# Kernel optimization log

Hardware: AMD Instinct MI355X
Metric: run time of the kernel (lower is better)

The kernel has to match this reference:

```python
import jax, jax.numpy as jnp
import numpy as np

B, IN_CAPS, IN_DIM = 64, 2048, 16
NUM_CAPS, OUT_DIM = 32, 16
NUM_ROUTING = 3


def squash(v, axis=-1):
    # scale = |v|^2 / (1 + |v|^2) / |v|  (faithful to source, no epsilon)
    s2 = jnp.sum(jnp.square(v), axis=axis, keepdims=True)
    scale = s2 / (1.0 + s2) / jnp.sqrt(s2)
    return scale * v


def setup_inputs() -> dict:
    key = jax.random.key(0)
    k1, k2 = jax.random.split(key)
    inputs = jax.random.normal(k1, (B, IN_CAPS, IN_DIM), dtype=jnp.float32)
    # glorot-ish scaled transform matrices
    W = jax.random.normal(k2, (IN_CAPS, NUM_CAPS, IN_DIM, OUT_DIM), dtype=jnp.float32) * 0.05
    return {"inputs": inputs, "W": W}


def reference(inputs, W):
    # Prediction vectors u_hat[b,i,k,:] = inputs[b,i,:] @ W[i,k,:,:]
    u_hat = jnp.einsum('bid,ikdo->biko', inputs, W)  # [B, I, K, O]
    # Routing logits b (per-batch; source initializes from zeros and accumulates agreement)
    b = jnp.zeros(u_hat.shape[:3], dtype=u_hat.dtype)  # [B, I, K]
    v = None
    for i in range(NUM_ROUTING):
        c = jax.nn.softmax(b, axis=2)                      # coupling coeffs over output caps K
        s = jnp.einsum('bik,biko->bko', c, u_hat)          # weighted sum over input caps I
        v = squash(s)                                      # [B, K, O]
        if i != NUM_ROUTING - 1:
            b = b + jnp.einsum('biko,bko->bik', u_hat, v)  # agreement update
    return v  # [B, NUM_CAPS, OUT_DIM]
```

## Files before the change

kernel.cpp:

```cpp
#include <hip/hip_runtime.h>
#include <math.h>
#include <stdint.h>

#define NB 64
#define NI 2048
#define NK 32
#define ND 16

typedef _Float16 h2t   __attribute__((ext_vector_type(2)));
typedef _Float16 f16x4 __attribute__((ext_vector_type(4)));
typedef float    f32x4 __attribute__((ext_vector_type(4)));

#if defined(__has_builtin)
#if __has_builtin(__builtin_amdgcn_global_load_lds)
#define HAVE_GLL 1
#endif
#endif
#ifndef HAVE_GLL
#define HAVE_GLL 0
#endif

static __device__ __forceinline__ uint32_t pack_h2(float a, float b) {
    h2t p; p.x = (_Float16)a; p.y = (_Float16)b;
    return __builtin_bit_cast(uint32_t, p);
}

static __device__ __forceinline__ float swz_xor16(float x) {
    int v = __builtin_amdgcn_ds_swizzle(__builtin_bit_cast(int, x), 0x401F);
    return __builtin_bit_cast(float, v);
}
static __device__ __forceinline__ float xreduce_o(float p) {
    p += swz_xor16(p);
    p += __shfl_xor(p, 32);
    return p;
}

__global__ __launch_bounds__(256)
void conv_w(const float* __restrict__ Wg, uint32_t* __restrict__ Wh)
{
    __shared__ float tile[32 * 264];
    const int i = blockIdx.x;
    const int t = threadIdx.x;
    const float4* src = (const float4*)(Wg + (size_t)i * 8192);
#pragma unroll
    for (int j = 0; j < 8; ++j) {
        const int f4 = t + j * 256;
        const int k  = f4 >> 6;
        const int r4 = f4 & 63;
        *(float4*)(&tile[k * 264 + r4 * 4]) = src[f4];
    }
    __syncthreads();
    const int T  = t >> 3;
    const int l0 = (t & 7) * 8;
    const float* s = tile + T * 264;
    uint2* dst = (uint2*)(Wh + (size_t)i * 4096) + T * 64 + l0;
#pragma unroll
    for (int n = 0; n < 8; ++n) {
        const int l = l0 + n;
        const int q = l >> 4, r = l & 15;
        uint2 u;
        u.x = pack_h2(s[(4 * q + 0) * 16 + r], s[(4 * q + 1) * 16 + r]);
        u.y = pack_h2(s[(4 * q + 2) * 16 + r], s[(4 * q + 3) * 16 + r]);
        dst[n] = u;
    }
}

__global__ __launch_bounds__(256)
void conv_x(const float* __restrict__ X, uint32_t* __restrict__ XT)
{
    const int g = blockIdx.x * 256 + threadIdx.x;
    const int b = g >> 11, i = g & 2047;
    const float4* src = (const float4*)(X + ((size_t)b * 2048 + i) * 16);
    const float4 f0 = src[0], f1 = src[1], f2 = src[2], f3 = src[3];
    uint4 o0, o1;
    o0.x = pack_h2(f0.x, f0.y); o0.y = pack_h2(f0.z, f0.w);
    o0.z = pack_h2(f1.x, f1.y); o0.w = pack_h2(f1.z, f1.w);
    o1.x = pack_h2(f2.x, f2.y); o1.y = pack_h2(f2.z, f2.w);
    o1.z = pack_h2(f3.x, f3.y); o1.w = pack_h2(f3.z, f3.w);
    uint4* dst = (uint4*)(XT + (size_t)i * 512 + b * 8);
    dst[0] = o0; dst[1] = o1;
}

template<int VMODE>
__global__ __launch_bounds__(256, 3)
void caps_pass_m(const uint32_t* __restrict__ XT,
                 const uint32_t* __restrict__ Wh,
                 const float* __restrict__ V,
                 float* __restrict__ part)
{
    constexpr int IC = 8;
    __shared__ uint32_t Ws[3][4096];
    __shared__ uint32_t Xs[1024];
    __shared__ float    Ep[2][4][16];

    const int t = threadIdx.x;
    const int l = t & 63;
    const int w = t >> 6;
    const int r = l & 15;
    const int q = l >> 4;

    const int wg     = blockIdx.x;
    const int xcd    = wg & 7;
    const int slot   = wg >> 3;
    const int ichunk = xcd * 32 + (slot >> 2);
    const int bg     = slot & 3;
    const int i0 = ichunk * IC;
    const int b0 = bg * 16;

    f32x4 s_acc[8];
#pragma unroll
    for (int tt = 0; tt < 8; ++tt) s_acc[tt] = (f32x4){0.f, 0.f, 0.f, 0.f};

    f32x4 v_r[8];
    if constexpr (VMODE == 1) {
#pragma unroll
        for (int tt = 0; tt < 8; ++tt)
            v_r[tt] = *(const f32x4*)(V + ((size_t)(b0 + r) * NK + (8 * w + tt)) * 16 + 4 * q);
    }

    {
        const int ig = t >> 5, uu = t & 31;
        uint4 v = *(const uint4*)(XT + (size_t)(i0 + ig) * 512 + b0 * 8 + uu * 4);
        *(uint4*)&Xs[ig * 128 + uu * 4] = v;
    }

#define STAGE_W(buf, tile)                                                     \
    {                                                                          \
        const size_t ibase_ = (size_t)(tile) * 4096;                           \
        _Pragma("unroll")                                                      \
        for (int j = 0; j < 4; ++j) {                                          \
            const int p = w * 4 + j;                                           \
            STAGE_ONE(buf, ibase_, p)                                          \
        }                                                                      \
    }
#if HAVE_GLL
#define STAGE_ONE(buf, ibase_, p)                                              \
    __builtin_amdgcn_global_load_lds(                                          \
        (const __attribute__((address_space(1))) void*)(Wh + ibase_ + (p) * 256 + l * 4), \
        (__attribute__((address_space(3))) void*)&Ws[buf][(p) * 256], 16, 0, 0);
#define BAR_W(n) asm volatile("s_waitcnt vmcnt(" #n ")\ns_barrier" ::: "memory");
#else
#define STAGE_ONE(buf, ibase_, p)                                              \
    ((uint4*)&Ws[buf][(p) * 256])[l] = *(const uint4*)(Wh + ibase_ + (p) * 256 + l * 4);
#define BAR_W(n) asm volatile("s_waitcnt vmcnt(0) lgkmcnt(0)\ns_barrier" ::: "memory");
#endif
#define BAR_E() asm volatile("s_waitcnt lgkmcnt(0)\ns_barrier" ::: "memory");

    __syncthreads();

    STAGE_W(0, i0)
    STAGE_W(1, i0 + 1)

    int cur = 0;
    for (int ii = 0; ii < IC; ++ii) {
        if (ii + 1 < IC) { BAR_W(4) } else { BAR_W(0) }

        if (ii + 2 < IC) {
            const int nslot = (cur + 2 >= 3) ? cur - 1 : cur + 2;
            STAGE_W(nslot, i0 + ii + 2)
        }

        const f16x4 xb = *(const f16x4*)&Xs[ii * 128 + r * 8 + q * 2];

        if constexpr (VMODE == 0) {
#pragma unroll
            for (int tt = 0; tt < 8; ++tt) {
                const f16x4 a = *(const f16x4*)&Ws[cur][(w * 8 + tt) * 128 + l * 2];
                s_acc[tt] = __builtin_amdgcn_mfma_f32_16x16x16f16(a, xb, s_acc[tt], 0, 0, 0);
            }
        } else {
            f32x4 um[8];
#pragma unroll
            for (int tt = 0; tt < 8; ++tt) {
                const f16x4 a = *(const f16x4*)&Ws[cur][(w * 8 + tt) * 128 + l * 2];
                um[tt] = __builtin_amdgcn_mfma_f32_16x16x16f16(
                    a, xb, (f32x4){0.f, 0.f, 0.f, 0.f}, 0, 0, 0);
            }
            float e[8];
            float esp = 0.f;
#pragma unroll
            for (int tt = 0; tt < 8; ++tt) {
                float p = um[tt][0] * v_r[tt][0];
                p = fmaf(um[tt][1], v_r[tt][1], p);
                p = fmaf(um[tt][2], v_r[tt][2], p);
                p = fmaf(um[tt][3], v_r[tt][3], p);
                p = xreduce_o(p);
                e[tt] = __expf(p);
                esp += e[tt];
            }
            if (q == 0) Ep[ii & 1][w][r] = esp;
            BAR_E();
            const float es = Ep[ii & 1][0][r] + Ep[ii & 1][1][r]
                           + Ep[ii & 1][2][r] + Ep[ii & 1][3][r];
            const float ci = __builtin_amdgcn_rcpf(es);
#pragma unroll
            for (int tt = 0; tt < 8; ++tt) {
                const float c = e[tt] * ci;
                s_acc[tt][0] = fmaf(c, um[tt][0], s_acc[tt][0]);
                s_acc[tt][1] = fmaf(c, um[tt][1], s_acc[tt][1]);
                s_acc[tt][2] = fmaf(c, um[tt][2], s_acc[tt][2]);
                s_acc[tt][3] = fmaf(c, um[tt][3], s_acc[tt][3]);
            }
        }
        cur = (cur == 2) ? 0 : cur + 1;
    }
#undef STAGE_W
#undef STAGE_ONE
#undef BAR_W
#undef BAR_E

    float* base = part + (size_t)(bg * 256 + ichunk) * 8192 + r * 512 + 4 * q;
#pragma unroll
    for (int tt = 0; tt < 8; ++tt) {
        float4 st = {s_acc[tt][0], s_acc[tt][1], s_acc[tt][2], s_acc[tt][3]};
        *(float4*)(base + (8 * w + tt) * 16) = st;
    }
}

template<int RMODE>
__global__ __launch_bounds__(256)
void caps_reduce(const float* __restrict__ part,
                 const float* __restrict__ S0red,
                 float* __restrict__ S0out,
                 float* __restrict__ Vout)
{
    __shared__ float red[4][64];
    const int t   = threadIdx.x;
    const int jl  = t & 63;
    const int qc  = t >> 6;
    const int jb  = blockIdx.x * 64;
    const int j   = jb + jl;
    const int bg  = j >> 13;
    const int loc = j & 8191;
    const float* p = part + ((size_t)(bg * 256 + qc * 64)) * 8192 + loc;
    float sum = 0.f;
#pragma unroll 8
    for (int ic = 0; ic < 64; ++ic) sum += p[(size_t)ic * 8192];
    red[qc][jl] = sum;
    __syncthreads();
    if (t < 64) {
        const int jj = jb + t;
        float total = red[0][t] + red[1][t] + red[2][t] + red[3][t];
        if constexpr (RMODE == 0) {
            S0out[jj] = total;
            float val = total * (1.0f / 32.0f);
            float sq = val * val;
#pragma unroll
            for (int mask = 8; mask >= 1; mask >>= 1) sq += __shfl_xor(sq, mask);
            const float sc = sqrtf(sq) / (1.0f + sq);
            Vout[jj] = val * sc;
        } else if constexpr (RMODE == 1) {
            float val0 = S0red[jj] * (1.0f / 32.0f);
            float sq0 = val0 * val0;
#pragma unroll
            for (int mask = 8; mask >= 1; mask >>= 1) sq0 += __shfl_xor(sq0, mask);
            const float sc0 = sqrtf(sq0) / (1.0f + sq0);
            float sq1 = total * total;
#pragma unroll
            for (int mask = 8; mask >= 1; mask >>= 1) sq1 += __shfl_xor(sq1, mask);
            const float sc1 = sqrtf(sq1) / (1.0f + sq1);
            Vout[jj] = fmaf(val0, sc0, total * sc1);
        } else {
            float sq = total * total;
#pragma unroll
            for (int mask = 8; mask >= 1; mask >>= 1) sq += __shfl_xor(sq, mask);
            const float sc = sqrtf(sq) / (1.0f + sq);
            Vout[jj] = total * sc;
        }
    }
}

template<int VMODE>
__global__ __launch_bounds__(256, 4)
void caps_pass_f32(const float* __restrict__ X,
                   const float* __restrict__ Wg,
                   const float* __restrict__ S0,
                   const float* __restrict__ S1,
                   float* __restrict__ Sout)
{
    constexpr int IC = 8;
    __shared__ float Ws[8192];
    __shared__ float Xs[2048];

    const int t   = threadIdx.x;
    const int kk  = t & 31;
    const int oh  = (t >> 5) & 1;
    const int bq4 = t >> 6;

    const int wg     = blockIdx.x;
    const int xcd    = wg & 7;
    const int slot   = wg >> 3;
    const int ichunk = xcd * 32 + (slot >> 2);
    const int bg     = slot & 3;
    const int i0 = ichunk * IC;
    const int b0 = bg * 16;

    float s_acc[4][8];
#pragma unroll
    for (int bb = 0; bb < 4; ++bb)
#pragma unroll
        for (int o = 0; o < 8; ++o) s_acc[bb][o] = 0.f;

    float v_r[4][8];
    if constexpr (VMODE >= 1) {
#pragma unroll
        for (int bb = 0; bb < 4; ++bb) {
            const int b = b0 + bq4 * 4 + bb;
            const float* p0 = S0 + ((size_t)b * NK + kk) * 16 + oh * 8;
            float4 a = *(const float4*)(p0);
            float4 c = *(const float4*)(p0 + 4);
            float val0[8] = {a.x,a.y,a.z,a.w,c.x,c.y,c.z,c.w};
            float sq0 = 0.f;
#pragma unroll
            for (int o = 0; o < 8; ++o) { val0[o] *= (1.0f/32.0f); sq0 = fmaf(val0[o], val0[o], sq0); }
            sq0 += __shfl_xor(sq0, 32);
            const float sc0 = sqrtf(sq0) / (1.0f + sq0);
#pragma unroll
            for (int o = 0; o < 8; ++o) v_r[bb][o] = val0[o] * sc0;
            if constexpr (VMODE == 2) {
                const float* p1 = S1 + ((size_t)b * NK + kk) * 16 + oh * 8;
                float4 a1 = *(const float4*)(p1);
                float4 c1 = *(const float4*)(p1 + 4);
                float val1[8] = {a1.x,a1.y,a1.z,a1.w,c1.x,c1.y,c1.z,c1.w};
                float sq1 = 0.f;
#pragma unroll
                for (int o = 0; o < 8; ++o) sq1 = fmaf(val1[o], val1[o], sq1);
                sq1 += __shfl_xor(sq1, 32);
                const float sc1 = sqrtf(sq1) / (1.0f + sq1);
#pragma unroll
                for (int o = 0; o < 8; ++o) v_r[bb][o] = fmaf(val1[o], sc1, v_r[bb][o]);
            }
        }
    }

    {
        const int xb   = t >> 4;
        const int xig  = t & 7;
        const int half = (t >> 3) & 1;
        const float* xp = X + (size_t)(b0 + xb) * (NI * ND) + (size_t)(i0 + xig) * ND + half * 8;
        float4 f0 = *(const float4*)(xp);
        float4 f1 = *(const float4*)(xp + 4);
        float vals[8] = {f0.x,f0.y,f0.z,f0.w,f1.x,f1.y,f1.z,f1.w};
        const int m = (xig & 7) << 3;
#pragma unroll
        for (int jj = 0; jj < 8; ++jj) {
            const int d = half * 8 + jj;
            Xs[xig * 256 + ((16 * d + xb) ^ m)] = vals[jj];
        }
    }

    for (int ii = 0; ii < IC; ++ii) {
        const int i = i0 + ii;
        __syncthreads();
        {
            const float4* wsrc = (const float4*)(Wg + (size_t)i * 8192);
#pragma unroll
            for (int j = 0; j < 8; ++j) {
                float4 val = wsrc[t + j * 256];
                const int k = (t >> 6) + 4 * j;
                ((float4*)Ws)[k * 64 + ((t & 63) ^ (k & 7))] = val;
            }
        }
        __syncthreads();

        const int xm = (ii & 7) << 3;
        float u[4][8];
        if constexpr (VMODE >= 1) {
#pragma unroll
            for (int bb = 0; bb < 4; ++bb)
#pragma unroll
                for (int o = 0; o < 8; ++o) u[bb][o] = 0.f;
        }
#pragma unroll
        for (int d = 0; d < 16; ++d) {
            const float4 x4 = *(const float4*)(&Xs[ii * 256 + ((16 * d + 4 * bq4) ^ xm)]);
            float wvv[8];
            {
                const float4 wA = ((const float4*)Ws)[kk * 64 + ((d * 4 + oh * 2)     ^ (kk & 7))];
                const float4 wB = ((const float4*)Ws)[kk * 64 + ((d * 4 + oh * 2 + 1) ^ (kk & 7))];
                wvv[0]=wA.x; wvv[1]=wA.y; wvv[2]=wA.z; wvv[3]=wA.w;
                wvv[4]=wB.x; wvv[5]=wB.y; wvv[6]=wB.z; wvv[7]=wB.w;
            }
            if constexpr (VMODE >= 1) {
#pragma unroll
                for (int o = 0; o < 8; ++o) {
                    u[0][o] = fmaf(x4.x, wvv[o], u[0][o]);
                    u[1][o] = fmaf(x4.y, wvv[o], u[1][o]);
                    u[2][o] = fmaf(x4.z, wvv[o], u[2][o]);
                    u[3][o] = fmaf(x4.w, wvv[o], u[3][o]);
                }
            } else {
#pragma unroll
                for (int o = 0; o < 8; ++o) {
                    s_acc[0][o] = fmaf(x4.x, wvv[o], s_acc[0][o]);
                    s_acc[1][o] = fmaf(x4.y, wvv[o], s_acc[1][o]);
                    s_acc[2][o] = fmaf(x4.z, wvv[o], s_acc[2][o]);
                    s_acc[3][o] = fmaf(x4.w, wvv[o], s_acc[3][o]);
                }
            }
        }

        if constexpr (VMODE >= 1) {
#pragma unroll
            for (int bb = 0; bb < 4; ++bb) {
                float lg = 0.f;
#pragma unroll
                for (int o = 0; o < 8; ++o) lg = fmaf(u[bb][o], v_r[bb][o], lg);
                lg += __shfl_xor(lg, 32);
                float m = lg;
#pragma unroll
                for (int mask = 16; mask >= 1; mask >>= 1)
                    m = fmaxf(m, __shfl_xor(m, mask));
                const float e = __expf(lg - m);
                float ssum = e;
#pragma unroll
                for (int mask = 16; mask >= 1; mask >>= 1)
                    ssum += __shfl_xor(ssum, mask);
                const float c = e / ssum;
#pragma unroll
                for (int o = 0; o < 8; ++o)
                    s_acc[bb][o] = fmaf(c, u[bb][o], s_acc[bb][o]);
            }
        }
    }

#pragma unroll
    for (int bb = 0; bb < 4; ++bb) {
        float* sp = Sout + ((size_t)(b0 + bq4 * 4 + bb) * NK + kk) * 16 + oh * 8;
#pragma unroll
        for (int o = 0; o < 8; ++o) atomicAdd(sp + o, s_acc[bb][o]);
    }
}

__global__ __launch_bounds__(256)
void squash_kernel(const float* __restrict__ S, float* __restrict__ Vout)
{
    const int idx = blockIdx.x * 256 + threadIdx.x;
    float val = S[idx];
    float sq = val * val;
#pragma unroll
    for (int mask = 8; mask >= 1; mask >>= 1) sq += __shfl_xor(sq, mask);
    const float sc = sqrtf(sq) / (1.0f + sq);
    Vout[idx] = val * sc;
}

extern "C" void kernel_launch(void* const* d_in, const int* in_sizes, int n_in,
                              void* d_out, int out_size, void* d_ws, size_t ws_size,
                              hipStream_t stream)
{
    const float* X  = (const float*)d_in[0];
    const float* Wg = (const float*)d_in[1];
    float* out = (float*)d_out;

    const size_t WHU  = (size_t)2048 * 4096;
    const size_t XHU  = (size_t)64 * 2048 * 8;
    const size_t PART = (size_t)1024 * 8192;
    const size_t need = (WHU + XHU) * 4 + (PART + 3 * 32768) * 4;

    const dim3 blk(256), pgrid(1024), rgrid(512);

    if (ws_size >= need) {
        uint32_t* Wh = (uint32_t*)d_ws;
        uint32_t* XT = Wh + WHU;
        float* part  = (float*)(XT + XHU);
        float* s0    = part + PART;
        float* v0    = s0 + 32768;
        float* v01   = v0 + 32768;

        conv_w<<<dim3(2048), blk, 0, stream>>>(Wg, Wh);
        conv_x<<<dim3(512),  blk, 0, stream>>>(X, XT);

        caps_pass_m<0><<<pgrid, blk, 0, stream>>>(XT, Wh, nullptr, part);
        caps_reduce<0><<<rgrid, blk, 0, stream>>>(part, nullptr, s0, v0);
        caps_pass_m<1><<<pgrid, blk, 0, stream>>>(XT, Wh, v0, part);
        caps_reduce<1><<<rgrid, blk, 0, stream>>>(part, s0, nullptr, v01);
        caps_pass_m<1><<<pgrid, blk, 0, stream>>>(XT, Wh, v01, part);
        caps_reduce<2><<<rgrid, blk, 0, stream>>>(part, nullptr, nullptr, out);
    } else {
        float* s0 = (float*)d_ws;
        float* s1 = s0 + 32768;
        float* s2 = s1 + 32768;
        hipMemsetAsync(d_ws, 0, (size_t)3 * 32768 * sizeof(float), stream);
        caps_pass_f32<0><<<pgrid, blk, 0, stream>>>(X, Wg, nullptr, nullptr, s0);
        caps_pass_f32<1><<<pgrid, blk, 0, stream>>>(X, Wg, s0, nullptr, s1);
        caps_pass_f32<2><<<pgrid, blk, 0, stream>>>(X, Wg, s0, s1, s2);
        squash_kernel<<<dim3(128), blk, 0, stream>>>(s2, out);
    }
}
```

Before: 115.5 us.

## Double input-capsule chunk per block and store fp16 partial sums

Each pass block now covers 16 input capsules instead of 8, which halves the grid and the number of partial-sum slices. Partials are packed to fp16 pairs, and the reduce kernel sums 32 slices of half2 values with two outputs per thread. The aim is to cut the partial write/read traffic and the reduce work. In exchange each block has a longer serial loop, occupancy is lowered to 2 blocks/CU, and fp16 partials lose precision.

Measured after the change: 96.75 us (median of 2 runs). -16.2%, faster.

```diff
diff --git a/kernel.cpp b/kernel.cpp
--- a/kernel.cpp
+++ b/kernel.cpp
@@ -82,15 +82,15 @@
 }
 
 template<int VMODE>
-__global__ __launch_bounds__(256, 3)
+__global__ __launch_bounds__(256, 2)
 void caps_pass_m(const uint32_t* __restrict__ XT,
                  const uint32_t* __restrict__ Wh,
                  const float* __restrict__ V,
-                 float* __restrict__ part)
-{
-    constexpr int IC = 8;
+                 uint32_t* __restrict__ part_h)
+{
+    constexpr int IC = 16;
     __shared__ uint32_t Ws[3][4096];
-    __shared__ uint32_t Xs[1024];
+    __shared__ uint32_t Xs[2048];
     __shared__ float    Ep[2][4][16];
 
     const int t = threadIdx.x;
@@ -102,7 +102,7 @@
     const int wg     = blockIdx.x;
     const int xcd    = wg & 7;
     const int slot   = wg >> 3;
-    const int ichunk = xcd * 32 + (slot >> 2);
+    const int ichunk = xcd * 16 + (slot >> 2);
     const int bg     = slot & 3;
     const int i0 = ichunk * IC;
     const int b0 = bg * 16;
@@ -119,9 +119,10 @@
     }
 
     {
-        const int ig = t >> 5, uu = t & 31;
-        uint4 v = *(const uint4*)(XT + (size_t)(i0 + ig) * 512 + b0 * 8 + uu * 4);
-        *(uint4*)&Xs[ig * 128 + uu * 4] = v;
+        const int ig = t >> 4, uu = t & 15;
+        const uint4* src = (const uint4*)(XT + (size_t)(i0 + ig) * 512 + b0 * 8);
+        *(uint4*)&Xs[ig * 128 + uu * 4]        = src[uu];
+        *(uint4*)&Xs[ig * 128 + (uu + 16) * 4] = src[uu + 16];
     }
 
 #define STAGE_W(buf, tile)                                                     \
@@ -209,63 +210,76 @@
 #undef BAR_W
 #undef BAR_E
 
-    float* base = part + (size_t)(bg * 256 + ichunk) * 8192 + r * 512 + 4 * q;
+    uint32_t* base = part_h + (size_t)(bg * 128 + ichunk) * 4096 + r * 256 + 2 * q;
 #pragma unroll
     for (int tt = 0; tt < 8; ++tt) {
-        float4 st = {s_acc[tt][0], s_acc[tt][1], s_acc[tt][2], s_acc[tt][3]};
-        *(float4*)(base + (8 * w + tt) * 16) = st;
+        uint2 st;
+        st.x = pack_h2(s_acc[tt][0], s_acc[tt][1]);
+        st.y = pack_h2(s_acc[tt][2], s_acc[tt][3]);
+        *(uint2*)(base + (8 * w + tt) * 8) = st;
     }
 }
 
 template<int RMODE>
 __global__ __launch_bounds__(256)
-void caps_reduce(const float* __restrict__ part,
+void caps_reduce(const uint32_t* __restrict__ part_h,
                  const float* __restrict__ S0red,
                  float* __restrict__ S0out,
                  float* __restrict__ Vout)
 {
-    __shared__ float red[4][64];
+    __shared__ float2 red[4][64];
     const int t   = threadIdx.x;
     const int jl  = t & 63;
     const int qc  = t >> 6;
     const int jb  = blockIdx.x * 64;
     const int j   = jb + jl;
-    const int bg  = j >> 13;
-    const int loc = j & 8191;
-    const float* p = part + ((size_t)(bg * 256 + qc * 64)) * 8192 + loc;
-    float sum = 0.f;
+    const int b   = j >> 8;
+    const int bg  = b >> 4;
+    const int loc = (b & 15) * 256 + (j & 255);
+    const uint32_t* p = part_h + ((size_t)(bg * 128 + qc * 32)) * 4096 + loc;
+    float sx = 0.f, sy = 0.f;
 #pragma unroll 8
-    for (int ic = 0; ic < 64; ++ic) sum += p[(size_t)ic * 8192];
-    red[qc][jl] = sum;
+    for (int ic = 0; ic < 32; ++ic) {
+        h2t v = __builtin_bit_cast(h2t, p[(size_t)ic * 4096]);
+        sx += (float)v.x; sy += (float)v.y;
+    }
+    red[qc][jl] = make_float2(sx, sy);
     __syncthreads();
     if (t < 64) {
         const int jj = jb + t;
-        float total = red[0][t] + red[1][t] + red[2][t] + red[3][t];
+        float2 a0 = red[0][t], a1 = red[1][t], a2 = red[2][t], a3 = red[3][t];
+        const float tx = a0.x + a1.x + a2.x + a3.x;
+        const float ty = a0.y + a1.y + a2.y + a3.y;
         if constexpr (RMODE == 0) {
-            S0out[jj] = total;
-            float val = total * (1.0f / 32.0f);
-            float sq = val * val;
-#pragma unroll
-            for (int mask = 8; mask >= 1; mask >>= 1) sq += __shfl_xor(sq, mask);
+            S0out[2 * jj]     = tx;
+            S0out[2 * jj + 1] = ty;
+            const float vx = tx * (1.0f / 32.0f), vy = ty * (1.0f / 32.0f);
+            float sq = vx * vx + vy * vy;
+#pragma unroll
+            for (int mask = 4; mask >= 1; mask >>= 1) sq += __shfl_xor(sq, mask);
             const float sc = sqrtf(sq) / (1.0f + sq);
-            Vout[jj] = val * sc;
+            Vout[2 * jj]     = vx * sc;
+            Vout[2 * jj + 1] = vy * sc;
         } else if constexpr (RMODE == 1) {
-            float val0 = S0red[jj] * (1.0f / 32.0f);
-            float sq0 = val0 * val0;
-#pragma unroll
-            for (int mask = 8; mask >= 1; mask >>= 1) sq0 += __shfl_xor(sq0, mask);
+            const float v0x = S0red[2 * jj] * (1.0f / 32.0f);
+            const float v0y = S0red[2 * jj + 1] * (1.0f / 32.0f);
+            float sq0 = v0x * v0x + v0y * v0y;
+#pragma unroll
+            for (int mask = 4; mask >= 1; mask >>= 1) sq0 += __shfl_xor(sq0, mask);
             const float sc0 = sqrtf(sq0) / (1.0f + sq0);
-            float sq1 = total * total;
-#pragma unroll
-            for (int mask = 8; mask >= 1; mask >>= 1) sq1 += __shfl_xor(sq1, mask);
+            float sq1 = tx * tx + ty * ty;
+#pragma unroll
+            for (int mask = 4; mask >= 1; mask >>= 1) sq1 += __shfl_xor(sq1, mask);
             const float sc1 = sqrtf(sq1) / (1.0f + sq1);
-            Vout[jj] = fmaf(val0, sc0, total * sc1);
+            Vout[2 * jj]     = fmaf(v0x, sc0, tx * sc1);
+            Vout[2 * jj + 1] = fmaf(v0y, sc0, ty * sc1);
         } else {
-            float sq = total * total;
-#pragma unroll
-            for (int mask = 8; mask >= 1; mask >>= 1) sq += __shfl_xor(sq, mask);
+            float sq = tx * tx + ty * ty;
+#pragma unroll
+            for (int mask = 4; mask >= 1; mask >>= 1) sq += __shfl_xor(sq, mask);
             const float sc = sqrtf(sq) / (1.0f + sq);
-            Vout[jj] = total * sc;
+            Vout[2 * jj]     = tx * sc;
+            Vout[2 * jj + 1] = ty * sc;
         }
     }
 }
@@ -452,20 +466,20 @@
     const float* Wg = (const float*)d_in[1];
     float* out = (float*)d_out;
 
-    const size_t WHU  = (size_t)2048 * 4096;
-    const size_t XHU  = (size_t)64 * 2048 * 8;
-    const size_t PART = (size_t)1024 * 8192;
-    const size_t need = (WHU + XHU) * 4 + (PART + 3 * 32768) * 4;
-
-    const dim3 blk(256), pgrid(1024), rgrid(512);
+    const size_t WHU   = (size_t)2048 * 4096;
+    const size_t XHU   = (size_t)64 * 2048 * 8;
+    const size_t PARTU = (size_t)512 * 4096;
+    const size_t need  = (WHU + XHU + PARTU) * 4 + 3 * 32768 * 4;
+
+    const dim3 blk(256), pgrid(512), rgrid(256);
 
     if (ws_size >= need) {
-        uint32_t* Wh = (uint32_t*)d_ws;
-        uint32_t* XT = Wh + WHU;
-        float* part  = (float*)(XT + XHU);
-        float* s0    = part + PART;
-        float* v0    = s0 + 32768;
-        float* v01   = v0 + 32768;
+        uint32_t* Wh   = (uint32_t*)d_ws;
+        uint32_t* XT   = Wh + WHU;
+        uint32_t* part = XT + XHU;
+        float* s0      = (float*)(part + PARTU);
+        float* v0      = s0 + 32768;
+        float* v01     = v0 + 32768;
 
         conv_w<<<dim3(2048), blk, 0, stream>>>(Wg, Wh);
         conv_x<<<dim3(512),  blk, 0, stream>>>(X, XT);
@@ -481,9 +495,9 @@
         float* s1 = s0 + 32768;
         float* s2 = s1 + 32768;
         hipMemsetAsync(d_ws, 0, (size_t)3 * 32768 * sizeof(float), stream);
-        caps_pass_f32<0><<<pgrid, blk, 0, stream>>>(X, Wg, nullptr, nullptr, s0);
-        caps_pass_f32<1><<<pgrid, blk, 0, stream>>>(X, Wg, s0, nullptr, s1);
-        caps_pass_f32<2><<<pgrid, blk, 0, stream>>>(X, Wg, s0, s1, s2);
+        caps_pass_f32<0><<<dim3(1024), blk, 0, stream>>>(X, Wg, nullptr, nullptr, s0);
+        caps_pass_f32<1><<<dim3(1024), blk, 0, stream>>>(X, Wg, s0, nullptr, s1);
+        caps_pass_f32<2><<<dim3(1024), blk, 0, stream>>>(X, Wg, s0, s1, s2);
         squash_kernel<<<dim3(128), blk, 0, stream>>>(s2, out);
     }
 }
```
